# Kernel optimization log

Measured on AMD Instinct MI355X. Metric: run time of the kernel, lower is better.

Reference implementation:

```python
import jax, jax.numpy as jnp
import numpy as np

N = 20000
E = 640000
IN_C, HID_C, OUT_C = 256, 256, 128
R = 8


def setup_inputs() -> dict:
    key = jax.random.key(0)
    ks = jax.random.split(key, 10)
    x = jax.random.normal(ks[0], (N, IN_C), dtype=jnp.float32)
    edge_index = jax.random.randint(ks[1], (2, E), 0, N, dtype=jnp.int64)
    edge_type = jax.random.randint(ks[2], (E,), 0, R, dtype=jnp.int64)
    s1 = 1.0 / np.sqrt(IN_C)
    s2 = 1.0 / np.sqrt(HID_C)
    W1 = jax.random.normal(ks[3], (R, IN_C, HID_C), dtype=jnp.float32) * s1
    root1 = jax.random.normal(ks[4], (IN_C, HID_C), dtype=jnp.float32) * s1
    b1 = jnp.zeros((HID_C,), dtype=jnp.float32)
    W2 = jax.random.normal(ks[5], (R, HID_C, OUT_C), dtype=jnp.float32) * s2
    root2 = jax.random.normal(ks[6], (HID_C, OUT_C), dtype=jnp.float32) * s2
    b2 = jnp.zeros((OUT_C,), dtype=jnp.float32)
    return {"x": x, "W1": W1, "root1": root1, "b1": b1,
            "W2": W2, "root2": root2, "b2": b2,
            "edge_index": edge_index, "edge_type": edge_type}


def _rgcn_conv(x, W, root, b, src, dst, etype):
    # Per-relation transform of ALL nodes: [R, N, out]
    t = jnp.einsum('ni,rio->rno', x, W)
    # Gather relation-specific messages per edge: [E, out]
    msg = t[etype, src]
    # Mean aggregation per (target node, relation), as in PyG RGCNConv (aggr='mean')
    comp = dst * R + etype  # composite segment id [E]
    cnt = jax.ops.segment_sum(jnp.ones_like(etype, dtype=x.dtype), comp,
                              num_segments=x.shape[0] * R)
    norm = 1.0 / jnp.maximum(cnt[comp], 1.0)
    agg = jax.ops.segment_sum(msg * norm[:, None], dst,
                              num_segments=x.shape[0])
    return agg + x @ root + b


def reference(x, W1, root1, b1, W2, root2, b2, edge_index, edge_type):
    src, dst = edge_index[0], edge_index[1]
    h = jax.nn.relu(_rgcn_conv(x, W1, root1, b1, src, dst, edge_type))
    return _rgcn_conv(h, W2, root2, b2, src, dst, edge_type)
```

## Files before the change

### kernel.cpp

```cpp
#include <hip/hip_runtime.h>

#define NN 20000
#define NE 640000
#define NR 8
#define NSEG (NN * NR)
#define KCAT 2304
#define CH1 256
#define CH2 128

typedef __attribute__((ext_vector_type(8))) short short8;
typedef __attribute__((ext_vector_type(4))) float f32x4;

#define AS_GLOBAL __attribute__((address_space(1)))
#define AS_LDS    __attribute__((address_space(3)))

__device__ __forceinline__ float bf2f(unsigned short u) {
    unsigned int x = ((unsigned int)u) << 16;
    return __builtin_bit_cast(float, x);
}
__device__ __forceinline__ unsigned short f2bf(float f) {
    unsigned int u = __builtin_bit_cast(unsigned int, f);
    u = (u + 0x7FFFu + ((u >> 16) & 1u)) >> 16;
    return (unsigned short)u;
}
__device__ __forceinline__ f32x4 cvt4(ushort4 v) {
    f32x4 r;
    r.x = bf2f(v.x); r.y = bf2f(v.y); r.z = bf2f(v.z); r.w = bf2f(v.w);
    return r;
}

__global__ void count_kernel(const int* __restrict__ dst, const int* __restrict__ et,
                             int* __restrict__ cnt) {
    int e = blockIdx.x * blockDim.x + threadIdx.x;
    if (e < NE) atomicAdd(&cnt[et[e] * NN + dst[e]], 1);
}

__global__ void scan1(const int* __restrict__ cnt, int* __restrict__ off,
                      int* __restrict__ bsum) {
    __shared__ int s[256];
    int i = blockIdx.x * 256 + threadIdx.x;
    int v = (i < NSEG) ? cnt[i] : 0;
    s[threadIdx.x] = v;
    __syncthreads();
    for (int d = 1; d < 256; d <<= 1) {
        int t = (threadIdx.x >= d) ? s[threadIdx.x - d] : 0;
        __syncthreads();
        s[threadIdx.x] += t;
        __syncthreads();
    }
    if (i < NSEG) off[i] = s[threadIdx.x] - v;
    if (threadIdx.x == 255) bsum[blockIdx.x] = s[255];
}

__global__ __launch_bounds__(1024) void scan2(int* __restrict__ bsum, int nb) {
    __shared__ int s[1024];
    int t = threadIdx.x;
    int v = (t < nb) ? bsum[t] : 0;
    s[t] = v;
    __syncthreads();
    for (int d = 1; d < 1024; d <<= 1) {
        int tv = (t >= d) ? s[t - d] : 0;
        __syncthreads();
        s[t] += tv;
        __syncthreads();
    }
    if (t < nb) bsum[t] = s[t] - v;
}

__global__ void scan3(int* __restrict__ off, const int* __restrict__ bsum,
                      int* __restrict__ cursor) {
    int i = blockIdx.x * 256 + threadIdx.x;
    if (i < NSEG) {
        int o = off[i] + bsum[blockIdx.x];
        off[i] = o;
        cursor[i] = o;
    }
}

__global__ void bucket_kernel(const int* __restrict__ src, const int* __restrict__ dst,
                              const int* __restrict__ et, int* __restrict__ cursor,
                              int* __restrict__ ss) {
    int e = blockIdx.x * blockDim.x + threadIdx.x;
    if (e < NE) {
        int p = atomicAdd(&cursor[et[e] * NN + dst[e]], 1);
        ss[p] = src[e];
    }
}

__global__ void cvt_bf16(const float* __restrict__ in, unsigned short* __restrict__ ob, int n4) {
    int i = blockIdx.x * blockDim.x + threadIdx.x;
    if (i < n4) {
        float4 v = reinterpret_cast<const float4*>(in)[i];
        ushort4 o;
        o.x = f2bf(v.x); o.y = f2bf(v.y); o.z = f2bf(v.z); o.w = f2bf(v.w);
        reinterpret_cast<ushort4*>(ob)[i] = o;
    }
}

__global__ void build_wt(const float* __restrict__ root, const float* __restrict__ W,
                         unsigned short* __restrict__ WT, int nout) {
    int i = blockIdx.x * 256 + threadIdx.x;
    if (i >= nout * KCAT) return;
    int n = i / KCAT, k = i - n * KCAT;
    float v;
    if (k < 256) v = root[(size_t)k * nout + n];
    else { int r = (k - 256) >> 8, kk = (k - 256) & 255; v = W[((size_t)r * 256 + kk) * nout + n]; }
    WT[(size_t)n * KCAT + k] = f2bf(v);
}

__global__ __launch_bounds__(256) void gather_all(const unsigned short* __restrict__ xb,
                                                  const int* __restrict__ ss,
                                                  const int* __restrict__ off,
                                                  const int* __restrict__ cnt,
                                                  unsigned short* __restrict__ A,
                                                  int n0, int rows) {
    int wid  = blockIdx.x * 4 + (threadIdx.x >> 6);
    int lane = threadIdx.x & 63;
    if (wid >= rows * (NR + 1)) return;
    int n = wid / (NR + 1);
    int j = wid - n * (NR + 1);
    if (j == 0) {
        reinterpret_cast<ushort4*>(A + (size_t)n * KCAT)[lane] =
            reinterpret_cast<const ushort4*>(xb + (size_t)(n0 + n) * 256)[lane];
        return;
    }
    int r    = j - 1;
    int idx  = r * NN + (n0 + n);
    int base = off[idx];
    int c    = cnt[idx];

    f32x4 a0 = {0.f, 0.f, 0.f, 0.f}, a1 = a0, a2 = a0, a3 = a0;
    int jj = 0;
    for (; jj + 4 <= c; jj += 4) {
        int s0 = ss[base + jj + 0];
        int s1 = ss[base + jj + 1];
        int s2 = ss[base + jj + 2];
        int s3 = ss[base + jj + 3];
        ushort4 v0 = reinterpret_cast<const ushort4*>(xb + (size_t)s0 * 256)[lane];
        ushort4 v1 = reinterpret_cast<const ushort4*>(xb + (size_t)s1 * 256)[lane];
        ushort4 v2 = reinterpret_cast<const ushort4*>(xb + (size_t)s2 * 256)[lane];
        ushort4 v3 = reinterpret_cast<const ushort4*>(xb + (size_t)s3 * 256)[lane];
        a0 += cvt4(v0); a1 += cvt4(v1); a2 += cvt4(v2); a3 += cvt4(v3);
    }
    int rem = c - jj;
    if (rem > 0) {
        int s0 = ss[base + jj + 0];
        int s1 = (rem > 1) ? ss[base + jj + 1] : s0;
        int s2 = (rem > 2) ? ss[base + jj + 2] : s0;
        ushort4 v0 = reinterpret_cast<const ushort4*>(xb + (size_t)s0 * 256)[lane];
        ushort4 v1 = (rem > 1) ? reinterpret_cast<const ushort4*>(xb + (size_t)s1 * 256)[lane] : make_ushort4(0,0,0,0);
        ushort4 v2 = (rem > 2) ? reinterpret_cast<const ushort4*>(xb + (size_t)s2 * 256)[lane] : make_ushort4(0,0,0,0);
        a0 += cvt4(v0);
        if (rem > 1) a1 += cvt4(v1);
        if (rem > 2) a2 += cvt4(v2);
    }
    f32x4 acc = (a0 + a1) + (a2 + a3);
    float inv = (c > 0) ? 1.f / (float)c : 0.f;
    ushort4 o;
    o.x = f2bf(acc.x * inv); o.y = f2bf(acc.y * inv);
    o.z = f2bf(acc.z * inv); o.w = f2bf(acc.w * inv);
    reinterpret_cast<ushort4*>(A + (size_t)n * KCAT + 256 + r * 256)[lane] = o;
}

template<int NOUT, int BN, bool RELU_BF16>
__global__ __launch_bounds__(256) void gemm_mfma(const unsigned short* __restrict__ A,
                                                 const unsigned short* __restrict__ BT,
                                                 const float* __restrict__ bias,
                                                 void* __restrict__ Cout,
                                                 int M, int mrow0) {
    constexpr int MI = (BN == 128) ? 4 : 2;
    __shared__ __align__(16) unsigned short As[128 * 32];
    __shared__ __align__(16) unsigned short Bs[BN * 32];
    const int tid  = threadIdx.x;
    const int lane = tid & 63;
    const int w    = tid >> 6;
    const int wr   = (BN == 128) ? (w >> 1) : w;
    const int wc   = (BN == 128) ? (w & 1) : 0;
    const int wrow = wr * (MI * 16);
    const int wcol = wc * 64;
    const int row0 = blockIdx.x * 128;
    const int col0 = blockIdx.y * BN;

    const int srow = lane >> 2;
    const int skk  = (lane & 3) * 8;
    int ra0 = row0 + w * 16 + srow;
    int ra1 = row0 + 64 + w * 16 + srow;
    ra0 = (ra0 < M) ? ra0 : (M - 1);
    ra1 = (ra1 < M) ? ra1 : (M - 1);
    const unsigned short* pa0 = A + (size_t)ra0 * KCAT + skk;
    const unsigned short* pa1 = A + (size_t)ra1 * KCAT + skk;
    const unsigned short* pb0 = BT + (size_t)(col0 + w * 16 + srow) * KCAT + skk;
    const unsigned short* pb1 = BT + (size_t)(col0 + 64 + w * 16 + srow) * KCAT + skk;
    unsigned short* lA0 = As + w * 512;
    unsigned short* lA1 = As + 2048 + w * 512;
    unsigned short* lB0 = Bs + w * 512;
    unsigned short* lB1 = Bs + 2048 + w * 512;

    f32x4 acc[MI][4] = {};
    const int fr = lane & 15;
    const int ka = (lane >> 4) * 8;

    for (int k0 = 0; k0 < KCAT; k0 += 32) {
        __builtin_amdgcn_global_load_lds((const AS_GLOBAL unsigned int*)(pa0 + k0),
                                         (AS_LDS unsigned int*)lA0, 16, 0, 0);
        __builtin_amdgcn_global_load_lds((const AS_GLOBAL unsigned int*)(pa1 + k0),
                                         (AS_LDS unsigned int*)lA1, 16, 0, 0);
        __builtin_amdgcn_global_load_lds((const AS_GLOBAL unsigned int*)(pb0 + k0),
                                         (AS_LDS unsigned int*)lB0, 16, 0, 0);
        if (BN == 128)
            __builtin_amdgcn_global_load_lds((const AS_GLOBAL unsigned int*)(pb1 + k0),
                                             (AS_LDS unsigned int*)lB1, 16, 0, 0);
        __syncthreads();

        short8 af[MI], bfrag[4];
        #pragma unroll
        for (int i = 0; i < MI; ++i)
            af[i] = *reinterpret_cast<const short8*>(&As[(wrow + i * 16 + fr) * 32 + ka]);
        #pragma unroll
        for (int i = 0; i < 4; ++i)
            bfrag[i] = *reinterpret_cast<const short8*>(&Bs[(wcol + i * 16 + fr) * 32 + ka]);
        #pragma unroll
        for (int mi = 0; mi < MI; ++mi)
            #pragma unroll
            for (int ni = 0; ni < 4; ++ni)
                acc[mi][ni] = __builtin_amdgcn_mfma_f32_16x16x32_bf16(af[mi], bfrag[ni], acc[mi][ni], 0, 0, 0);
        __syncthreads();
    }

    #pragma unroll
    for (int mi = 0; mi < MI; ++mi) {
        #pragma unroll
        for (int q = 0; q < 4; ++q) {
            int gm = row0 + wrow + mi * 16 + (lane >> 4) * 4 + q;
            if (gm >= M) continue;
            #pragma unroll
            for (int ni = 0; ni < 4; ++ni) {
                int gn = col0 + wcol + ni * 16 + fr;
                float v = acc[mi][ni][q] + bias[gn];
                if (RELU_BF16) {
                    v = fmaxf(v, 0.f);
                    ((unsigned short*)Cout)[(size_t)(mrow0 + gm) * NOUT + gn] = f2bf(v);
                } else {
                    ((float*)Cout)[(size_t)(mrow0 + gm) * NOUT + gn] = v;
                }
            }
        }
    }
}

extern "C" void kernel_launch(void* const* d_in, const int* in_sizes, int n_in,
                              void* d_out, int out_size, void* d_ws, size_t ws_size,
                              hipStream_t stream) {
    const float* x     = (const float*)d_in[0];
    const float* W1    = (const float*)d_in[1];
    const float* root1 = (const float*)d_in[2];
    const float* b1    = (const float*)d_in[3];
    const float* W2    = (const float*)d_in[4];
    const float* root2 = (const float*)d_in[5];
    const float* b2    = (const float*)d_in[6];
    const int*   ei    = (const int*)d_in[7];
    const int*   et    = (const int*)d_in[8];
    const int* src = ei;
    const int* dst = ei + NE;
    float* out = (float*)d_out;

    char* ws = (char*)d_ws;
    int*            cnt    = (int*)(ws + 0);
    int*            off    = (int*)(ws + 640000);
    int*            cursor = (int*)(ws + 1280000);
    int*            bsum   = (int*)(ws + 1920000);
    int*            ss     = (int*)(ws + 1923072);
    unsigned short* x_bf   = (unsigned short*)(ws + 4483072);
    unsigned short* h_bf   = (unsigned short*)(ws + 14723072);
    unsigned short* W1T    = (unsigned short*)(ws + 24963072);
    unsigned short* W2T    = (unsigned short*)(ws + 26142720);
    unsigned short* A      = (unsigned short*)(ws + 26732544);

    size_t availA = (ws_size > 26732544) ? ws_size - 26732544 : 0;
    int rowsC = (int)((availA / ((size_t)KCAT * 2)));
    if (rowsC > NN) rowsC = NN;
    if (rowsC >= 256) rowsC &= ~127;
    if (rowsC < 1) rowsC = 1;

    const int NB = (NSEG + 255) / 256;

    hipMemsetAsync(cnt, 0, (size_t)NSEG * 4, stream);
    count_kernel<<<(NE + 255) / 256, 256, 0, stream>>>(dst, et, cnt);
    scan1<<<NB, 256, 0, stream>>>(cnt, off, bsum);
    scan2<<<1, 1024, 0, stream>>>(bsum, NB);
    scan3<<<NB, 256, 0, stream>>>(off, bsum, cursor);
    bucket_kernel<<<(NE + 255) / 256, 256, 0, stream>>>(src, dst, et, cursor, ss);

    build_wt<<<(CH1 * KCAT + 255) / 256, 256, 0, stream>>>(root1, W1, W1T, CH1);
    build_wt<<<(CH2 * KCAT + 255) / 256, 256, 0, stream>>>(root2, W2, W2T, CH2);
    cvt_bf16<<<(NN * 256 / 4 + 255) / 256, 256, 0, stream>>>(x, x_bf, NN * 256 / 4);

    for (int n0 = 0; n0 < NN; n0 += rowsC) {
        int rows = (NN - n0 < rowsC) ? (NN - n0) : rowsC;
        gather_all<<<(rows * (NR + 1) + 3) / 4, 256, 0, stream>>>(x_bf, ss, off, cnt, A, n0, rows);
        dim3 g((rows + 127) / 128, CH1 / 128);
        gemm_mfma<CH1, 128, true><<<g, 256, 0, stream>>>(A, W1T, b1, h_bf, rows, n0);
    }
    for (int n0 = 0; n0 < NN; n0 += rowsC) {
        int rows = (NN - n0 < rowsC) ? (NN - n0) : rowsC;
        gather_all<<<(rows * (NR + 1) + 3) / 4, 256, 0, stream>>>(h_bf, ss, off, cnt, A, n0, rows);
        dim3 g((rows + 127) / 128, CH2 / 64);
        gemm_mfma<CH2, 64, false><<<g, 256, 0, stream>>>(A, W2T, b2, out, rows, n0);
    }
}
```

Baseline: 453.0 us.

## Read self features directly in GEMM, gather two relations per wave, merge prologue kernels

The GEMM now loads the root (self) K-slice straight from the bf16 node feature buffer, so gather no longer copies each node's own features into the concatenated A matrix. A shrinks from 2304 to 2048 columns. The gather kernel has each wave handle two relations for a node with interleaved loads, which raises memory-level parallelism and cuts the wave count. The x-to-bf16 conversion is merged with edge counting, and the two weight-transpose launches become one, to reduce launch overhead. In exchange, the GEMM loop gains a per-iteration pointer select, and the interleaved gather loop is more branchy.

```diff
diff --git a/kernel.cpp b/kernel.cpp
--- a/kernel.cpp
+++ b/kernel.cpp
@@ -5,6 +5,7 @@
 #define NR 8
 #define NSEG (NN * NR)
 #define KCAT 2304
+#define KA   2048
 #define CH1 256
 #define CH2 128
 
@@ -28,11 +29,21 @@
     r.x = bf2f(v.x); r.y = bf2f(v.y); r.z = bf2f(v.z); r.w = bf2f(v.w);
     return r;
 }
-
-__global__ void count_kernel(const int* __restrict__ dst, const int* __restrict__ et,
-                             int* __restrict__ cnt) {
-    int e = blockIdx.x * blockDim.x + threadIdx.x;
-    if (e < NE) atomicAdd(&cnt[et[e] * NN + dst[e]], 1);
+__device__ __forceinline__ ushort4 ldrow(const unsigned short* xb, int s, int lane) {
+    return reinterpret_cast<const ushort4*>(xb + (size_t)s * 256)[lane];
+}
+
+__global__ void prologue1(const int* __restrict__ dst, const int* __restrict__ et,
+                          int* __restrict__ cnt,
+                          const float* __restrict__ x, unsigned short* __restrict__ xbf) {
+    int gid = blockIdx.x * 256 + threadIdx.x;
+    if (gid < NN * 64) {
+        float4 v = reinterpret_cast<const float4*>(x)[gid];
+        ushort4 o;
+        o.x = f2bf(v.x); o.y = f2bf(v.y); o.z = f2bf(v.z); o.w = f2bf(v.w);
+        reinterpret_cast<ushort4*>(xbf)[gid] = o;
+    }
+    if (gid < NE) atomicAdd(&cnt[et[gid] * NN + dst[gid]], 1);
 }
 
 __global__ void scan1(const int* __restrict__ cnt, int* __restrict__ off,
@@ -87,25 +98,20 @@
     }
 }
 
-__global__ void cvt_bf16(const float* __restrict__ in, unsigned short* __restrict__ ob, int n4) {
-    int i = blockIdx.x * blockDim.x + threadIdx.x;
-    if (i < n4) {
-        float4 v = reinterpret_cast<const float4*>(in)[i];
-        ushort4 o;
-        o.x = f2bf(v.x); o.y = f2bf(v.y); o.z = f2bf(v.z); o.w = f2bf(v.w);
-        reinterpret_cast<ushort4*>(ob)[i] = o;
-    }
-}
-
-__global__ void build_wt(const float* __restrict__ root, const float* __restrict__ W,
-                         unsigned short* __restrict__ WT, int nout) {
+__global__ void build_wt_all(const float* __restrict__ root1, const float* __restrict__ W1,
+                             const float* __restrict__ root2, const float* __restrict__ W2,
+                             unsigned short* __restrict__ W1T, unsigned short* __restrict__ W2T) {
     int i = blockIdx.x * 256 + threadIdx.x;
-    if (i >= nout * KCAT) return;
-    int n = i / KCAT, k = i - n * KCAT;
-    float v;
-    if (k < 256) v = root[(size_t)k * nout + n];
-    else { int r = (k - 256) >> 8, kk = (k - 256) & 255; v = W[((size_t)r * 256 + kk) * nout + n]; }
-    WT[(size_t)n * KCAT + k] = f2bf(v);
+    if (i < CH1 * KCAT) {
+        int n = i / KCAT, k = i - n * KCAT;
+        float v = (k < 256) ? root1[(size_t)k * CH1 + n] : W1[(size_t)(k - 256) * CH1 + n];
+        W1T[(size_t)n * KCAT + k] = f2bf(v);
+    } else if (i < (CH1 + CH2) * KCAT) {
+        int j = i - CH1 * KCAT;
+        int n = j / KCAT, k = j - n * KCAT;
+        float v = (k < 256) ? root2[(size_t)k * CH2 + n] : W2[(size_t)(k - 256) * CH2 + n];
+        W2T[(size_t)n * KCAT + k] = f2bf(v);
+    }
 }
 
 __global__ __launch_bounds__(256) void gather_all(const unsigned short* __restrict__ xb,
@@ -116,54 +122,57 @@
                                                   int n0, int rows) {
     int wid  = blockIdx.x * 4 + (threadIdx.x >> 6);
     int lane = threadIdx.x & 63;
-    if (wid >= rows * (NR + 1)) return;
-    int n = wid / (NR + 1);
-    int j = wid - n * (NR + 1);
-    if (j == 0) {
-        reinterpret_cast<ushort4*>(A + (size_t)n * KCAT)[lane] =
-            reinterpret_cast<const ushort4*>(xb + (size_t)(n0 + n) * 256)[lane];
-        return;
-    }
-    int r    = j - 1;
-    int idx  = r * NN + (n0 + n);
-    int base = off[idx];
-    int c    = cnt[idx];
-
-    f32x4 a0 = {0.f, 0.f, 0.f, 0.f}, a1 = a0, a2 = a0, a3 = a0;
-    int jj = 0;
-    for (; jj + 4 <= c; jj += 4) {
-        int s0 = ss[base + jj + 0];
-        int s1 = ss[base + jj + 1];
-        int s2 = ss[base + jj + 2];
-        int s3 = ss[base + jj + 3];
-        ushort4 v0 = reinterpret_cast<const ushort4*>(xb + (size_t)s0 * 256)[lane];
-        ushort4 v1 = reinterpret_cast<const ushort4*>(xb + (size_t)s1 * 256)[lane];
-        ushort4 v2 = reinterpret_cast<const ushort4*>(xb + (size_t)s2 * 256)[lane];
-        ushort4 v3 = reinterpret_cast<const ushort4*>(xb + (size_t)s3 * 256)[lane];
-        a0 += cvt4(v0); a1 += cvt4(v1); a2 += cvt4(v2); a3 += cvt4(v3);
-    }
-    int rem = c - jj;
-    if (rem > 0) {
-        int s0 = ss[base + jj + 0];
-        int s1 = (rem > 1) ? ss[base + jj + 1] : s0;
-        int s2 = (rem > 2) ? ss[base + jj + 2] : s0;
-        ushort4 v0 = reinterpret_cast<const ushort4*>(xb + (size_t)s0 * 256)[lane];
-        ushort4 v1 = (rem > 1) ? reinterpret_cast<const ushort4*>(xb + (size_t)s1 * 256)[lane] : make_ushort4(0,0,0,0);
-        ushort4 v2 = (rem > 2) ? reinterpret_cast<const ushort4*>(xb + (size_t)s2 * 256)[lane] : make_ushort4(0,0,0,0);
-        a0 += cvt4(v0);
-        if (rem > 1) a1 += cvt4(v1);
-        if (rem > 2) a2 += cvt4(v2);
-    }
-    f32x4 acc = (a0 + a1) + (a2 + a3);
-    float inv = (c > 0) ? 1.f / (float)c : 0.f;
-    ushort4 o;
-    o.x = f2bf(acc.x * inv); o.y = f2bf(acc.y * inv);
-    o.z = f2bf(acc.z * inv); o.w = f2bf(acc.w * inv);
-    reinterpret_cast<ushort4*>(A + (size_t)n * KCAT + 256 + r * 256)[lane] = o;
+    if (wid >= rows * 4) return;
+    int n  = wid >> 2;
+    int r0 = (wid & 3) * 2;
+    int idx0  = r0 * NN + (n0 + n);
+    int idx1  = idx0 + NN;
+    int base0 = off[idx0], c0 = cnt[idx0];
+    int base1 = off[idx1], c1 = cnt[idx1];
+
+    f32x4 z = {0.f, 0.f, 0.f, 0.f};
+    f32x4 a0 = z, a1 = z, a2 = z, a3 = z;
+    f32x4 b0 = z, b1 = z, b2 = z, b3 = z;
+    int j0 = 0, j1 = 0;
+    while (j0 < c0 || j1 < c1) {
+        int m0 = c0 - j0; m0 = (m0 > 4) ? 4 : m0;
+        int m1 = c1 - j1; m1 = (m1 > 4) ? 4 : m1;
+        ushort4 v00, v01, v02, v03, v10, v11, v12, v13;
+        if (m0 > 0) v00 = ldrow(xb, ss[base0 + j0 + 0], lane);
+        if (m0 > 1) v01 = ldrow(xb, ss[base0 + j0 + 1], lane);
+        if (m0 > 2) v02 = ldrow(xb, ss[base0 + j0 + 2], lane);
+        if (m0 > 3) v03 = ldrow(xb, ss[base0 + j0 + 3], lane);
+        if (m1 > 0) v10 = ldrow(xb, ss[base1 + j1 + 0], lane);
+        if (m1 > 1) v11 = ldrow(xb, ss[base1 + j1 + 1], lane);
+        if (m1 > 2) v12 = ldrow(xb, ss[base1 + j1 + 2], lane);
+        if (m1 > 3) v13 = ldrow(xb, ss[base1 + j1 + 3], lane);
+        if (m0 > 0) a0 += cvt4(v00);
+        if (m0 > 1) a1 += cvt4(v01);
+        if (m0 > 2) a2 += cvt4(v02);
+        if (m0 > 3) a3 += cvt4(v03);
+        if (m1 > 0) b0 += cvt4(v10);
+        if (m1 > 1) b1 += cvt4(v11);
+        if (m1 > 2) b2 += cvt4(v12);
+        if (m1 > 3) b3 += cvt4(v13);
+        j0 += m0; j1 += m1;
+    }
+    f32x4 s0 = (a0 + a1) + (a2 + a3);
+    f32x4 s1 = (b0 + b1) + (b2 + b3);
+    float inv0 = (c0 > 0) ? 1.f / (float)c0 : 0.f;
+    float inv1 = (c1 > 0) ? 1.f / (float)c1 : 0.f;
+    ushort4 o0, o1;
+    o0.x = f2bf(s0.x * inv0); o0.y = f2bf(s0.y * inv0);
+    o0.z = f2bf(s0.z * inv0); o0.w = f2bf(s0.w * inv0);
+    o1.x = f2bf(s1.x * inv1); o1.y = f2bf(s1.y * inv1);
+    o1.z = f2bf(s1.z * inv1); o1.w = f2bf(s1.w * inv1);
+    unsigned short* arow = A + (size_t)n * KA + r0 * 256;
+    reinterpret_cast<ushort4*>(arow)[lane] = o0;
+    reinterpret_cast<ushort4*>(arow + 256)[lane] = o1;
 }
 
 template<int NOUT, int BN, bool RELU_BF16>
 __global__ __launch_bounds__(256) void gemm_mfma(const unsigned short* __restrict__ A,
+                                                 const unsigned short* __restrict__ Xsrc,
                                                  const unsigned short* __restrict__ BT,
                                                  const float* __restrict__ bias,
                                                  void* __restrict__ Cout,
@@ -187,8 +196,10 @@
     int ra1 = row0 + 64 + w * 16 + srow;
     ra0 = (ra0 < M) ? ra0 : (M - 1);
     ra1 = (ra1 < M) ? ra1 : (M - 1);
-    const unsigned short* pa0 = A + (size_t)ra0 * KCAT + skk;
-    const unsigned short* pa1 = A + (size_t)ra1 * KCAT + skk;
+    const unsigned short* pax0 = Xsrc + (size_t)(mrow0 + ra0) * 256 + skk;
+    const unsigned short* pax1 = Xsrc + (size_t)(mrow0 + ra1) * 256 + skk;
+    const unsigned short* paa0 = A + (size_t)ra0 * KA + skk - 256;
+    const unsigned short* paa1 = A + (size_t)ra1 * KA + skk - 256;
     const unsigned short* pb0 = BT + (size_t)(col0 + w * 16 + srow) * KCAT + skk;
     const unsigned short* pb1 = BT + (size_t)(col0 + 64 + w * 16 + srow) * KCAT + skk;
     unsigned short* lA0 = As + w * 512;
@@ -201,9 +212,11 @@
     const int ka = (lane >> 4) * 8;
 
     for (int k0 = 0; k0 < KCAT; k0 += 32) {
-        __builtin_amdgcn_global_load_lds((const AS_GLOBAL unsigned int*)(pa0 + k0),
+        const unsigned short* p0 = (k0 < 256) ? (pax0 + k0) : (paa0 + k0);
+        const unsigned short* p1 = (k0 < 256) ? (pax1 + k0) : (paa1 + k0);
+        __builtin_amdgcn_global_load_lds((const AS_GLOBAL unsigned int*)p0,
                                          (AS_LDS unsigned int*)lA0, 16, 0, 0);
-        __builtin_amdgcn_global_load_lds((const AS_GLOBAL unsigned int*)(pa1 + k0),
+        __builtin_amdgcn_global_load_lds((const AS_GLOBAL unsigned int*)p1,
                                          (AS_LDS unsigned int*)lA1, 16, 0, 0);
         __builtin_amdgcn_global_load_lds((const AS_GLOBAL unsigned int*)(pb0 + k0),
                                          (AS_LDS unsigned int*)lB0, 16, 0, 0);
@@ -277,7 +290,7 @@
     unsigned short* A      = (unsigned short*)(ws + 26732544);
 
     size_t availA = (ws_size > 26732544) ? ws_size - 26732544 : 0;
-    int rowsC = (int)((availA / ((size_t)KCAT * 2)));
+    int rowsC = (int)(availA / ((size_t)KA * 2));
     if (rowsC > NN) rowsC = NN;
     if (rowsC >= 256) rowsC &= ~127;
     if (rowsC < 1) rowsC = 1;
@@ -285,26 +298,23 @@
     const int NB = (NSEG + 255) / 256;
 
     hipMemsetAsync(cnt, 0, (size_t)NSEG * 4, stream);
-    count_kernel<<<(NE + 255) / 256, 256, 0, stream>>>(dst, et, cnt);
+    prologue1<<<(NN * 64 + 255) / 256, 256, 0, stream>>>(dst, et, cnt, x, x_bf);
     scan1<<<NB, 256, 0, stream>>>(cnt, off, bsum);
     scan2<<<1, 1024, 0, stream>>>(bsum, NB);
     scan3<<<NB, 256, 0, stream>>>(off, bsum, cursor);
     bucket_kernel<<<(NE + 255) / 256, 256, 0, stream>>>(src, dst, et, cursor, ss);
-
-    build_wt<<<(CH1 * KCAT + 255) / 256, 256, 0, stream>>>(root1, W1, W1T, CH1);
-    build_wt<<<(CH2 * KCAT + 255) / 256, 256, 0, stream>>>(root2, W2, W2T, CH2);
-    cvt_bf16<<<(NN * 256 / 4 + 255) / 256, 256, 0, stream>>>(x, x_bf, NN * 256 / 4);
+    build_wt_all<<<((CH1 + CH2) * KCAT + 255) / 256, 256, 0, stream>>>(root1, W1, root2, W2, W1T, W2T);
 
     for (int n0 = 0; n0 < NN; n0 += rowsC) {
         int rows = (NN - n0 < rowsC) ? (NN - n0) : rowsC;
-        gather_all<<<(rows * (NR + 1) + 3) / 4, 256, 0, stream>>>(x_bf, ss, off, cnt, A, n0, rows);
+        gather_all<<<rows, 256, 0, stream>>>(x_bf, ss, off, cnt, A, n0, rows);
         dim3 g((rows + 127) / 128, CH1 / 128);
-        gemm_mfma<CH1, 128, true><<<g, 256, 0, stream>>>(A, W1T, b1, h_bf, rows, n0);
+        gemm_mfma<CH1, 128, true><<<g, 256, 0, stream>>>(A, x_bf, W1T, b1, h_bf, rows, n0);
     }
     for (int n0 = 0; n0 < NN; n0 += rowsC) {
         int rows = (NN - n0 < rowsC) ? (NN - n0) : rowsC;
-        gather_all<<<(rows * (NR + 1) + 3) / 4, 256, 0, stream>>>(h_bf, ss, off, cnt, A, n0, rows);
+        gather_all<<<rows, 256, 0, stream>>>(h_bf, ss, off, cnt, A, n0, rows);
         dim3 g((rows + 127) / 128, CH2 / 64);
-        gemm_mfma<CH2, 64, false><<<g, 256, 0, stream>>>(A, W2T, b2, out, rows, n0);
-    }
-}
+        gemm_mfma<CH2, 64, false><<<g, 256, 0, stream>>>(A, h_bf, W2T, b2, out, rows, n0);
+    }
+}
```

After: 489.9 us. 1.08x slower.

## Read root features directly in GEMM, fuse prologue kernels, shrink GEMM tiles

Applied to the files above, without the earlier changes.

The GEMM now loads the root-feature K-slice straight from the bf16 node features instead of from a copy in the concatenated A buffer. This removes the copy pass in gather_all and shrinks A to 2048 columns. The bf16 conversion of x is fused into the edge-count kernel, and the two weight-transpose kernels are merged into one launch. The GEMM tile height drops from 128 to 64 rows, with a 2x2 wave layout for both layers, so more blocks cover the 20000 rows. The trade-off is a per-iteration pointer select in the K loop and a smaller per-block tile.

```diff
diff --git a/kernel.cpp b/kernel.cpp
--- a/kernel.cpp
+++ b/kernel.cpp
@@ -5,6 +5,7 @@
 #define NR 8
 #define NSEG (NN * NR)
 #define KCAT 2304
+#define KA   2048
 #define CH1 256
 #define CH2 128
 
@@ -29,10 +30,17 @@
     return r;
 }
 
-__global__ void count_kernel(const int* __restrict__ dst, const int* __restrict__ et,
-                             int* __restrict__ cnt) {
-    int e = blockIdx.x * blockDim.x + threadIdx.x;
-    if (e < NE) atomicAdd(&cnt[et[e] * NN + dst[e]], 1);
+__global__ void prologue1(const int* __restrict__ dst, const int* __restrict__ et,
+                          int* __restrict__ cnt,
+                          const float* __restrict__ x, unsigned short* __restrict__ xbf) {
+    int gid = blockIdx.x * 256 + threadIdx.x;
+    if (gid < NN * 64) {
+        float4 v = reinterpret_cast<const float4*>(x)[gid];
+        ushort4 o;
+        o.x = f2bf(v.x); o.y = f2bf(v.y); o.z = f2bf(v.z); o.w = f2bf(v.w);
+        reinterpret_cast<ushort4*>(xbf)[gid] = o;
+    }
+    if (gid < NE) atomicAdd(&cnt[et[gid] * NN + dst[gid]], 1);
 }
 
 __global__ void scan1(const int* __restrict__ cnt, int* __restrict__ off,
@@ -87,25 +95,20 @@
     }
 }
 
-__global__ void cvt_bf16(const float* __restrict__ in, unsigned short* __restrict__ ob, int n4) {
-    int i = blockIdx.x * blockDim.x + threadIdx.x;
-    if (i < n4) {
-        float4 v = reinterpret_cast<const float4*>(in)[i];
-        ushort4 o;
-        o.x = f2bf(v.x); o.y = f2bf(v.y); o.z = f2bf(v.z); o.w = f2bf(v.w);
-        reinterpret_cast<ushort4*>(ob)[i] = o;
-    }
-}
-
-__global__ void build_wt(const float* __restrict__ root, const float* __restrict__ W,
-                         unsigned short* __restrict__ WT, int nout) {
+__global__ void build_wt_all(const float* __restrict__ root1, const float* __restrict__ W1,
+                             const float* __restrict__ root2, const float* __restrict__ W2,
+                             unsigned short* __restrict__ W1T, unsigned short* __restrict__ W2T) {
     int i = blockIdx.x * 256 + threadIdx.x;
-    if (i >= nout * KCAT) return;
-    int n = i / KCAT, k = i - n * KCAT;
-    float v;
-    if (k < 256) v = root[(size_t)k * nout + n];
-    else { int r = (k - 256) >> 8, kk = (k - 256) & 255; v = W[((size_t)r * 256 + kk) * nout + n]; }
-    WT[(size_t)n * KCAT + k] = f2bf(v);
+    if (i < CH1 * KCAT) {
+        int n = i / KCAT, k = i - n * KCAT;
+        float v = (k < 256) ? root1[(size_t)k * CH1 + n] : W1[(size_t)(k - 256) * CH1 + n];
+        W1T[(size_t)n * KCAT + k] = f2bf(v);
+    } else if (i < (CH1 + CH2) * KCAT) {
+        int j = i - CH1 * KCAT;
+        int n = j / KCAT, k = j - n * KCAT;
+        float v = (k < 256) ? root2[(size_t)k * CH2 + n] : W2[(size_t)(k - 256) * CH2 + n];
+        W2T[(size_t)n * KCAT + k] = f2bf(v);
+    }
 }
 
 __global__ __launch_bounds__(256) void gather_all(const unsigned short* __restrict__ xb,
@@ -116,20 +119,15 @@
                                                   int n0, int rows) {
     int wid  = blockIdx.x * 4 + (threadIdx.x >> 6);
     int lane = threadIdx.x & 63;
-    if (wid >= rows * (NR + 1)) return;
-    int n = wid / (NR + 1);
-    int j = wid - n * (NR + 1);
-    if (j == 0) {
-        reinterpret_cast<ushort4*>(A + (size_t)n * KCAT)[lane] =
-            reinterpret_cast<const ushort4*>(xb + (size_t)(n0 + n) * 256)[lane];
-        return;
-    }
-    int r    = j - 1;
+    if (wid >= rows * NR) return;
+    int n = wid >> 3;
+    int r = wid & 7;
     int idx  = r * NN + (n0 + n);
     int base = off[idx];
     int c    = cnt[idx];
 
-    f32x4 a0 = {0.f, 0.f, 0.f, 0.f}, a1 = a0, a2 = a0, a3 = a0;
+    f32x4 z = {0.f, 0.f, 0.f, 0.f};
+    f32x4 a0 = z, a1 = z, a2 = z, a3 = z;
     int jj = 0;
     for (; jj + 4 <= c; jj += 4) {
         int s0 = ss[base + jj + 0];
@@ -159,26 +157,27 @@
     ushort4 o;
     o.x = f2bf(acc.x * inv); o.y = f2bf(acc.y * inv);
     o.z = f2bf(acc.z * inv); o.w = f2bf(acc.w * inv);
-    reinterpret_cast<ushort4*>(A + (size_t)n * KCAT + 256 + r * 256)[lane] = o;
-}
-
-template<int NOUT, int BN, bool RELU_BF16>
+    reinterpret_cast<ushort4*>(A + (size_t)n * KA + r * 256)[lane] = o;
+}
+
+template<int NOUT, int BM, int BN, bool RELU_BF16>
 __global__ __launch_bounds__(256) void gemm_mfma(const unsigned short* __restrict__ A,
+                                                 const unsigned short* __restrict__ Xsrc,
                                                  const unsigned short* __restrict__ BT,
                                                  const float* __restrict__ bias,
                                                  void* __restrict__ Cout,
                                                  int M, int mrow0) {
-    constexpr int MI = (BN == 128) ? 4 : 2;
-    __shared__ __align__(16) unsigned short As[128 * 32];
+    constexpr int MI = BM / 32;
+    constexpr int NI = BN / 32;
+    __shared__ __align__(16) unsigned short As[BM * 32];
     __shared__ __align__(16) unsigned short Bs[BN * 32];
     const int tid  = threadIdx.x;
     const int lane = tid & 63;
     const int w    = tid >> 6;
-    const int wr   = (BN == 128) ? (w >> 1) : w;
-    const int wc   = (BN == 128) ? (w & 1) : 0;
+    const int wr   = w >> 1, wc = w & 1;
     const int wrow = wr * (MI * 16);
-    const int wcol = wc * 64;
-    const int row0 = blockIdx.x * 128;
+    const int wcol = wc * (NI * 16);
+    const int row0 = blockIdx.x * BM;
     const int col0 = blockIdx.y * BN;
 
     const int srow = lane >> 2;
@@ -187,8 +186,10 @@
     int ra1 = row0 + 64 + w * 16 + srow;
     ra0 = (ra0 < M) ? ra0 : (M - 1);
     ra1 = (ra1 < M) ? ra1 : (M - 1);
-    const unsigned short* pa0 = A + (size_t)ra0 * KCAT + skk;
-    const unsigned short* pa1 = A + (size_t)ra1 * KCAT + skk;
+    const unsigned short* pax0 = Xsrc + (size_t)(mrow0 + ra0) * 256 + skk;
+    const unsigned short* pax1 = Xsrc + (size_t)(mrow0 + ra1) * 256 + skk;
+    const unsigned short* paa0 = A + (size_t)ra0 * KA + skk - 256;
+    const unsigned short* paa1 = A + (size_t)ra1 * KA + skk - 256;
     const unsigned short* pb0 = BT + (size_t)(col0 + w * 16 + srow) * KCAT + skk;
     const unsigned short* pb1 = BT + (size_t)(col0 + 64 + w * 16 + srow) * KCAT + skk;
     unsigned short* lA0 = As + w * 512;
@@ -196,15 +197,19 @@
     unsigned short* lB0 = Bs + w * 512;
     unsigned short* lB1 = Bs + 2048 + w * 512;
 
-    f32x4 acc[MI][4] = {};
+    f32x4 acc[MI][NI] = {};
     const int fr = lane & 15;
     const int ka = (lane >> 4) * 8;
 
     for (int k0 = 0; k0 < KCAT; k0 += 32) {
-        __builtin_amdgcn_global_load_lds((const AS_GLOBAL unsigned int*)(pa0 + k0),
+        const unsigned short* p0 = (k0 < 256) ? (pax0 + k0) : (paa0 + k0);
+        __builtin_amdgcn_global_load_lds((const AS_GLOBAL unsigned int*)p0,
                                          (AS_LDS unsigned int*)lA0, 16, 0, 0);
-        __builtin_amdgcn_global_load_lds((const AS_GLOBAL unsigned int*)(pa1 + k0),
-                                         (AS_LDS unsigned int*)lA1, 16, 0, 0);
+        if (BM == 128) {
+            const unsigned short* p1 = (k0 < 256) ? (pax1 + k0) : (paa1 + k0);
+            __builtin_amdgcn_global_load_lds((const AS_GLOBAL unsigned int*)p1,
+                                             (AS_LDS unsigned int*)lA1, 16, 0, 0);
+        }
         __builtin_amdgcn_global_load_lds((const AS_GLOBAL unsigned int*)(pb0 + k0),
                                          (AS_LDS unsigned int*)lB0, 16, 0, 0);
         if (BN == 128)
@@ -212,17 +217,17 @@
                                              (AS_LDS unsigned int*)lB1, 16, 0, 0);
         __syncthreads();
 
-        short8 af[MI], bfrag[4];
+        short8 af[MI], bfrag[NI];
         #pragma unroll
         for (int i = 0; i < MI; ++i)
             af[i] = *reinterpret_cast<const short8*>(&As[(wrow + i * 16 + fr) * 32 + ka]);
         #pragma unroll
-        for (int i = 0; i < 4; ++i)
+        for (int i = 0; i < NI; ++i)
             bfrag[i] = *reinterpret_cast<const short8*>(&Bs[(wcol + i * 16 + fr) * 32 + ka]);
         #pragma unroll
         for (int mi = 0; mi < MI; ++mi)
             #pragma unroll
-            for (int ni = 0; ni < 4; ++ni)
+            for (int ni = 0; ni < NI; ++ni)
                 acc[mi][ni] = __builtin_amdgcn_mfma_f32_16x16x32_bf16(af[mi], bfrag[ni], acc[mi][ni], 0, 0, 0);
         __syncthreads();
     }
@@ -234,7 +239,7 @@
             int gm = row0 + wrow + mi * 16 + (lane >> 4) * 4 + q;
             if (gm >= M) continue;
             #pragma unroll
-            for (int ni = 0; ni < 4; ++ni) {
+            for (int ni = 0; ni < NI; ++ni) {
                 int gn = col0 + wcol + ni * 16 + fr;
                 float v = acc[mi][ni][q] + bias[gn];
                 if (RELU_BF16) {
@@ -277,7 +282,7 @@
     unsigned short* A      = (unsigned short*)(ws + 26732544);
 
     size_t availA = (ws_size > 26732544) ? ws_size - 26732544 : 0;
-    int rowsC = (int)((availA / ((size_t)KCAT * 2)));
+    int rowsC = (int)(availA / ((size_t)KA * 2));
     if (rowsC > NN) rowsC = NN;
     if (rowsC >= 256) rowsC &= ~127;
     if (rowsC < 1) rowsC = 1;
@@ -285,26 +290,23 @@
     const int NB = (NSEG + 255) / 256;
 
     hipMemsetAsync(cnt, 0, (size_t)NSEG * 4, stream);
-    count_kernel<<<(NE + 255) / 256, 256, 0, stream>>>(dst, et, cnt);
+    prologue1<<<(NN * 64 + 255) / 256, 256, 0, stream>>>(dst, et, cnt, x, x_bf);
     scan1<<<NB, 256, 0, stream>>>(cnt, off, bsum);
     scan2<<<1, 1024, 0, stream>>>(bsum, NB);
     scan3<<<NB, 256, 0, stream>>>(off, bsum, cursor);
     bucket_kernel<<<(NE + 255) / 256, 256, 0, stream>>>(src, dst, et, cursor, ss);
-
-    build_wt<<<(CH1 * KCAT + 255) / 256, 256, 0, stream>>>(root1, W1, W1T, CH1);
-    build_wt<<<(CH2 * KCAT + 255) / 256, 256, 0, stream>>>(root2, W2, W2T, CH2);
-    cvt_bf16<<<(NN * 256 / 4 + 255) / 256, 256, 0, stream>>>(x, x_bf, NN * 256 / 4);
+    build_wt_all<<<((CH1 + CH2) * KCAT + 255) / 256, 256, 0, stream>>>(root1, W1, root2, W2, W1T, W2T);
 
     for (int n0 = 0; n0 < NN; n0 += rowsC) {
         int rows = (NN - n0 < rowsC) ? (NN - n0) : rowsC;
-        gather_all<<<(rows * (NR + 1) + 3) / 4, 256, 0, stream>>>(x_bf, ss, off, cnt, A, n0, rows);
-        dim3 g((rows + 127) / 128, CH1 / 128);
-        gemm_mfma<CH1, 128, true><<<g, 256, 0, stream>>>(A, W1T, b1, h_bf, rows, n0);
+        gather_all<<<(rows * NR + 3) / 4, 256, 0, stream>>>(x_bf, ss, off, cnt, A, n0, rows);
+        dim3 g((rows + 63) / 64, CH1 / 128);
+        gemm_mfma<CH1, 64, 128, true><<<g, 256, 0, stream>>>(A, x_bf, W1T, b1, h_bf, rows, n0);
     }
     for (int n0 = 0; n0 < NN; n0 += rowsC) {
         int rows = (NN - n0 < rowsC) ? (NN - n0) : rowsC;
-        gather_all<<<(rows * (NR + 1) + 3) / 4, 256, 0, stream>>>(h_bf, ss, off, cnt, A, n0, rows);
-        dim3 g((rows + 127) / 128, CH2 / 64);
-        gemm_mfma<CH2, 64, false><<<g, 256, 0, stream>>>(A, W2T, b2, out, rows, n0);
-    }
-}
+        gather_all<<<(rows * NR + 3) / 4, 256, 0, stream>>>(h_bf, ss, off, cnt, A, n0, rows);
+        dim3 g((rows + 63) / 64, CH2 / 64);
+        gemm_mfma<CH2, 64, 64, false><<<g, 256, 0, stream>>>(A, h_bf, W2T, b2, out, rows, n0);
+    }
+}
```

Result: faster. 408.4 us (-9.8%).
